# Optimization experiments

Measured on AMD Instinct MI355X. Metric: run time of the kernel, lower is better.

The kernel has to match this reference:

```python
import jax, jax.numpy as jnp
import numpy as np

HEADS = 16
EPS = 1e-5

def _ln(x, w, b):
    # LayerNorm over last axis (per-head dim s), torch default eps=1e-5
    mu = jnp.mean(x, axis=-1, keepdims=True)
    var = jnp.var(x, axis=-1, keepdims=True)
    return (x - mu) * jax.lax.rsqrt(var + EPS) * w + b

def setup_inputs() -> dict:
    key = jax.random.key(0)
    ks = jax.random.split(key, 6)
    b, t, e = 4, 2048, 1024
    sc = 1.0 / np.sqrt(e)  # keep weight magnitudes sane
    return {
        "x": jax.random.normal(ks[0], (b, t, e), jnp.float32),
        "Wk": jax.random.normal(ks[1], (e, e), jnp.float32) * sc,
        "Wq": jax.random.normal(ks[2], (e, e), jnp.float32) * sc,
        "Wv": jax.random.normal(ks[3], (e, e), jnp.float32) * sc,
        "Wu": jax.random.normal(ks[4], (e, e), jnp.float32) * sc,
        "kln_w": jnp.ones((e // HEADS,), jnp.float32),
        "kln_b": jnp.zeros((e // HEADS,), jnp.float32),
        "qln_w": jnp.ones((e // HEADS,), jnp.float32),
        "qln_b": jnp.zeros((e // HEADS,), jnp.float32),
    }

def reference(x, Wk, Wq, Wv, Wu, kln_w, kln_b, qln_w, qln_b):
    b, t, e = x.shape
    h = HEADS
    s = e // h
    scale = 1.0 / np.sqrt(s)
    # nn.Linear(emb, emb, bias=False): y = x @ W.T
    k = (x @ Wk.T).reshape(b, t, h, s)
    q = (x @ Wq.T).reshape(b, t, h, s)
    v = (x @ Wv.T).reshape(b, t, h, s)
    # kqnorm: per-head LayerNorm on keys and queries
    k = _ln(k, kln_w, kln_b)
    q = _ln(q, qln_w, qln_b)
    # scores: (b, h, t, t)
    w = jnp.einsum('bihd,bjhd->bhij', q, k) * scale
    # causal mask: zero out strictly-upper-triangular (future) positions
    causal = jnp.tril(jnp.ones((t, t), bool))
    w = jnp.where(causal, w, -jnp.inf)
    p = jax.nn.softmax(w, axis=-1)
    out = jnp.einsum('bhij,bjhd->bihd', p, v).reshape(b, t, e)
    return out @ Wu.T
```

## Files before the change

### kernel.cpp

```cpp
#include <hip/hip_runtime.h>
#include <math.h>

#define EMB 1024
#define TSEQ 2048
#define NBATCH 4
#define NHEAD 16
#define HDIM 64
#define MROWS (NBATCH * TSEQ)
#define KPAD 72

typedef __attribute__((ext_vector_type(8))) short bf16x8;
typedef __attribute__((ext_vector_type(4))) float f32x4;
typedef __attribute__((ext_vector_type(8))) unsigned short u16x8;
typedef __attribute__((ext_vector_type(4))) unsigned short u16x4;

typedef __attribute__((address_space(1))) const void gas_cv;
typedef __attribute__((address_space(3))) void las_v;

__device__ __forceinline__ void gload_lds16(const void* g, void* l) {
  __builtin_amdgcn_global_load_lds((gas_cv*)g, (las_v*)l, 16, 0, 0);
}

__device__ __forceinline__ unsigned short f2bf(float f) {
  unsigned int x = __float_as_uint(f);
  unsigned int r = x + 0x7fffu + ((x >> 16) & 1u);
  return (unsigned short)(r >> 16);
}
__device__ __forceinline__ float bf2f(unsigned short h) {
  return __uint_as_float((unsigned int)h << 16);
}

__global__ __launch_bounds__(256) void decomp_kernel(
    const float* __restrict__ x, const float* __restrict__ Wk,
    const float* __restrict__ Wq, const float* __restrict__ Wv,
    const float* __restrict__ Wu,
    unsigned short* __restrict__ xh, unsigned short* __restrict__ xl,
    unsigned short* __restrict__ wkh, unsigned short* __restrict__ wkl,
    unsigned short* __restrict__ wqh, unsigned short* __restrict__ wql,
    unsigned short* __restrict__ wvh, unsigned short* __restrict__ wvl,
    unsigned short* __restrict__ wuh, unsigned short* __restrict__ wul) {
  const int v = blockIdx.x * blockDim.x + threadIdx.x;
  const float* src;
  unsigned short *dh, *dl;
  size_t off;
  if (v < (1 << 20)) {
    src = x; dh = xh; dl = xl; off = (size_t)v << 3;
  } else {
    const int wv = v - (1 << 20);
    const int ws_ = wv >> 17;
    off = (size_t)(wv & 131071) << 3;
    if (ws_ == 0) { src = Wk; dh = wkh; dl = wkl; }
    else if (ws_ == 1) { src = Wq; dh = wqh; dl = wql; }
    else if (ws_ == 2) { src = Wv; dh = wvh; dl = wvl; }
    else { src = Wu; dh = wuh; dl = wul; }
  }
  const float4 f0 = *(const float4*)(src + off);
  const float4 f1 = *(const float4*)(src + off + 4);
  const float fv[8] = {f0.x, f0.y, f0.z, f0.w, f1.x, f1.y, f1.z, f1.w};
  u16x8 h, l;
#pragma unroll
  for (int i = 0; i < 8; ++i) {
    const unsigned short hb = f2bf(fv[i]);
    h[i] = hb;
    l[i] = f2bf(fv[i] - bf2f(hb));
  }
  *(u16x8*)(dh + off) = h;
  *(u16x8*)(dl + off) = l;
}

__device__ __forceinline__ void gemm3_core(
    const unsigned short* __restrict__ Ah,
    const unsigned short* __restrict__ Bh, const unsigned short* __restrict__ Bl,
    int bm, int bn, f32x4 acc[4][4]) {
  __shared__ __align__(16) unsigned short As[128][64];
  __shared__ __align__(16) unsigned short Bs[128][64];
  const int tid = threadIdx.x;
  const int lane = tid & 63;
  const int w = tid >> 6;
  const int lq = lane & 15;
  const int g = lane >> 4;
  const int wrO = (w >> 1) << 6;
  const int wcO = (w & 1) << 6;
  const int srow = (w << 5) + (lane >> 3);
  const int scbs = ((lane & 7) ^ (srow & 7)) << 3;
  const int xsw = lq & 7;

  const size_t aoff0 = (size_t)(bm + srow) * EMB + scbs;
  const size_t boff0 = (size_t)(bn + srow) * EMB + scbs;

  for (int s = 0; s < 32; ++s) {
    const int p = s >> 4;
    const int kt = s & 15;
    const unsigned short* Bsrc = (p == 0) ? Bh : Bl;
    const size_t ko = (size_t)(kt << 6);
    __syncthreads();
#pragma unroll
    for (int u = 0; u < 4; ++u) {
      gload_lds16(Ah + aoff0 + ko + (size_t)(u << 3) * EMB,
                  &As[(w << 5) + (u << 3)][0]);
      gload_lds16(Bsrc + boff0 + ko + (size_t)(u << 3) * EMB,
                  &Bs[(w << 5) + (u << 3)][0]);
    }
    __syncthreads();

    bf16x8 af[4][2], bf[4][2];
#pragma unroll
    for (int m = 0; m < 4; ++m)
#pragma unroll
      for (int kk = 0; kk < 2; ++kk) {
        af[m][kk] = *(const bf16x8*)&As[wrO + (m << 4) + lq]
                                      [(((kk << 2) + g) ^ xsw) << 3];
        bf[m][kk] = *(const bf16x8*)&Bs[wcO + (m << 4) + lq]
                                      [(((kk << 2) + g) ^ xsw) << 3];
      }
#pragma unroll
    for (int kk = 0; kk < 2; ++kk)
#pragma unroll
      for (int m = 0; m < 4; ++m)
#pragma unroll
        for (int nb = 0; nb < 4; ++nb)
          acc[m][nb] = __builtin_amdgcn_mfma_f32_16x16x32_bf16(
              af[m][kk], bf[nb][kk], acc[m][nb], 0, 0, 0);
  }
}

__global__ __launch_bounds__(256, 2) void gemm3_qkv_kernel(
    const unsigned short* __restrict__ xh,
    const unsigned short* __restrict__ wkh, const unsigned short* __restrict__ wkl,
    const unsigned short* __restrict__ wqh, const unsigned short* __restrict__ wql,
    const unsigned short* __restrict__ wvh, const unsigned short* __restrict__ wvl,
    unsigned short* __restrict__ kb16, unsigned short* __restrict__ qb16,
    unsigned short* __restrict__ vb16,
    const float* __restrict__ klnw, const float* __restrict__ klnb,
    const float* __restrict__ qlnw, const float* __restrict__ qlnb) {
  const int sel = blockIdx.y >> 3;
  const int bm = blockIdx.x << 7;
  const int bn = (blockIdx.y & 7) << 7;
  const unsigned short* Bh = sel == 0 ? wkh : sel == 1 ? wqh : wvh;
  const unsigned short* Bl = sel == 0 ? wkl : sel == 1 ? wql : wvl;

  f32x4 acc[4][4];
#pragma unroll
  for (int m = 0; m < 4; ++m)
#pragma unroll
    for (int nb = 0; nb < 4; ++nb) acc[m][nb] = (f32x4){0.f, 0.f, 0.f, 0.f};

  gemm3_core(xh, Bh, Bl, bm, bn, acc);

  const int lane = threadIdx.x & 63;
  const int w = threadIdx.x >> 6;
  const int lq = lane & 15;
  const int g = lane >> 4;
  const int wrO = (w >> 1) << 6;
  const int wcO = (w & 1) << 6;

  if (sel < 2) {
    unsigned short* C = sel == 0 ? kb16 : qb16;
    const float* lw = sel == 0 ? klnw : qlnw;
    const float* lb = sel == 0 ? klnb : qlnb;
    float wd[4], bd[4];
#pragma unroll
    for (int nb = 0; nb < 4; ++nb) {
      wd[nb] = lw[(nb << 4) + lq];
      bd[nb] = lb[(nb << 4) + lq];
    }
#pragma unroll
    for (int m = 0; m < 4; ++m) {
      const int r0 = bm + wrO + (m << 4) + (g << 2);
#pragma unroll
      for (int j = 0; j < 4; ++j) {
        float s = acc[m][0][j] + acc[m][1][j] + acc[m][2][j] + acc[m][3][j];
        s += __shfl_xor(s, 1, 64); s += __shfl_xor(s, 2, 64);
        s += __shfl_xor(s, 4, 64); s += __shfl_xor(s, 8, 64);
        const float mu = s * (1.f / 64.f);
        float v2 = 0.f;
#pragma unroll
        for (int nb = 0; nb < 4; ++nb) {
          const float d = acc[m][nb][j] - mu;
          v2 = fmaf(d, d, v2);
        }
        v2 += __shfl_xor(v2, 1, 64); v2 += __shfl_xor(v2, 2, 64);
        v2 += __shfl_xor(v2, 4, 64); v2 += __shfl_xor(v2, 8, 64);
        const float inv = rsqrtf(v2 * (1.f / 64.f) + 1e-5f);
#pragma unroll
        for (int nb = 0; nb < 4; ++nb) {
          const float val = (acc[m][nb][j] - mu) * inv * wd[nb] + bd[nb];
          C[(size_t)(r0 + j) * EMB + bn + wcO + (nb << 4) + lq] = f2bf(val);
        }
      }
    }
  } else {
#pragma unroll
    for (int m = 0; m < 4; ++m) {
      const int r0 = bm + wrO + (m << 4) + (g << 2);
      const int bb = r0 >> 11;
      const int tl = r0 & 2047;
#pragma unroll
      for (int nb = 0; nb < 4; ++nb) {
        const int n = bn + wcO + (nb << 4) + lq;
        const int hh = n >> 6;
        const int dd = n & 63;
        u16x4 pk;
#pragma unroll
        for (int j = 0; j < 4; ++j) pk[j] = f2bf(acc[m][nb][j]);
        *(u16x4*)(vb16 + ((((size_t)(bb << 4) + hh) << 6) + dd) * TSEQ + tl) = pk;
      }
    }
  }
}

__global__ __launch_bounds__(256, 2) void gemm3_out_kernel(
    const unsigned short* __restrict__ ah,
    const unsigned short* __restrict__ wuh, const unsigned short* __restrict__ wul,
    float* __restrict__ C) {
  const int bm = blockIdx.x << 7;
  const int bn = blockIdx.y << 7;
  f32x4 acc[4][4];
#pragma unroll
  for (int m = 0; m < 4; ++m)
#pragma unroll
    for (int nb = 0; nb < 4; ++nb) acc[m][nb] = (f32x4){0.f, 0.f, 0.f, 0.f};

  gemm3_core(ah, wuh, wul, bm, bn, acc);

  const int lane = threadIdx.x & 63;
  const int w = threadIdx.x >> 6;
  const int lq = lane & 15;
  const int g = lane >> 4;
  const int wrO = (w >> 1) << 6;
  const int wcO = (w & 1) << 6;
#pragma unroll
  for (int m = 0; m < 4; ++m) {
    const int r0 = bm + wrO + (m << 4) + (g << 2);
#pragma unroll
    for (int nb = 0; nb < 4; ++nb) {
      const int c = bn + wcO + (nb << 4) + lq;
#pragma unroll
      for (int j = 0; j < 4; ++j) C[(size_t)(r0 + j) * EMB + c] = acc[m][nb][j];
    }
  }
}

#define SCL2E 0.1803368801111244f

__global__ __launch_bounds__(256, 2) void attn_kernel(
    const unsigned short* __restrict__ Qg, const unsigned short* __restrict__ Kg,
    const unsigned short* __restrict__ Vt,
    unsigned short* __restrict__ Oh, unsigned short* __restrict__ Ol) {
  __shared__ __align__(16) unsigned short Ks[64][KPAD];
  __shared__ __align__(16) unsigned short Vs[64][KPAD];
  __shared__ __align__(16) unsigned short Ps[4][16][KPAD];
  const int tid = threadIdx.x;
  const int lane = tid & 63;
  const int w = tid >> 6;
  const int lq = lane & 15;
  const int g = lane >> 4;
  const int qt = (int)(gridDim.x - 1 - blockIdx.x);
  const int bh = blockIdx.y;
  const int bb = bh >> 4;
  const int hh = bh & 15;
  const int q0 = qt << 6;
  const unsigned short* Qb = Qg + ((size_t)bb * TSEQ) * EMB + hh * HDIM;
  const unsigned short* Kb = Kg + ((size_t)bb * TSEQ) * EMB + hh * HDIM;
  const unsigned short* Vb = Vt + (size_t)bh * HDIM * TSEQ;
  unsigned short* Ohb = Oh + ((size_t)bb * TSEQ) * EMB + hh * HDIM;
  unsigned short* Olb = Ol + ((size_t)bb * TSEQ) * EMB + hh * HDIM;

  bf16x8 qf0, qf1;
  {
    const unsigned short* qp = Qb + (size_t)(q0 + (w << 4) + lq) * EMB + (g << 3);
    qf0 = *(const bf16x8*)(qp);
    qf1 = *(const bf16x8*)(qp + 32);
  }

  f32x4 o[4];
#pragma unroll
  for (int nb = 0; nb < 4; ++nb) o[nb] = (f32x4){0.f, 0.f, 0.f, 0.f};
  float mrun = -3.0e38f;
  float lrun = 0.f;
  const int qg_row = q0 + (w << 4) + lq;

  const int skey = tid >> 2;
  const int schunk = (tid & 3) << 4;

  for (int t = 0; t <= qt; ++t) {
    const int k0 = t << 6;
    {
      const unsigned short* kp = Kb + (size_t)(k0 + skey) * EMB + schunk;
      *(bf16x8*)&Ks[skey][schunk] = *(const bf16x8*)kp;
      *(bf16x8*)&Ks[skey][schunk + 8] = *(const bf16x8*)(kp + 8);
      const unsigned short* vp = Vb + (size_t)skey * TSEQ + k0 + schunk;
      *(bf16x8*)&Vs[skey][schunk] = *(const bf16x8*)vp;
      *(bf16x8*)&Vs[skey][schunk + 8] = *(const bf16x8*)(vp + 8);
    }
    __syncthreads();

    f32x4 sacc[4];
#pragma unroll
    for (int mb = 0; mb < 4; ++mb) sacc[mb] = (f32x4){0.f, 0.f, 0.f, 0.f};
    __builtin_amdgcn_s_setprio(1);
#pragma unroll
    for (int mb = 0; mb < 4; ++mb) {
      const bf16x8 ka0 = *(const bf16x8*)&Ks[(mb << 4) + lq][(g << 3)];
      const bf16x8 ka1 = *(const bf16x8*)&Ks[(mb << 4) + lq][(g << 3) + 32];
      sacc[mb] = __builtin_amdgcn_mfma_f32_16x16x32_bf16(ka0, qf0, sacc[mb], 0, 0, 0);
      sacc[mb] = __builtin_amdgcn_mfma_f32_16x16x32_bf16(ka1, qf1, sacc[mb], 0, 0, 0);
    }
    __builtin_amdgcn_s_setprio(0);

    const bool diag = (t == qt);
    float pv[16];
    float pm = -3.0e38f;
#pragma unroll
    for (int mb = 0; mb < 4; ++mb)
#pragma unroll
      for (int r = 0; r < 4; ++r) {
        float s = sacc[mb][r] * SCL2E;
        if (diag && (k0 + (mb << 4) + (g << 2) + r) > qg_row) s = -3.0e38f;
        pv[(mb << 2) + r] = s;
        pm = fmaxf(pm, s);
      }
    pm = fmaxf(pm, __shfl_xor(pm, 16, 64));
    pm = fmaxf(pm, __shfl_xor(pm, 32, 64));

    const bool skip = __all(pm <= mrun);
    const float mnew = skip ? mrun : fmaxf(mrun, pm);
    float ls = 0.f;
#pragma unroll
    for (int i = 0; i < 16; ++i) {
      const float p = exp2f(pv[i] - mnew);
      pv[i] = p;
      ls += p;
    }
    ls += __shfl_xor(ls, 16, 64);
    ls += __shfl_xor(ls, 32, 64);
    if (skip) {
      lrun += ls;
    } else {
      const float corr = exp2f(mrun - mnew);
      mrun = mnew;
      lrun = lrun * corr + ls;
      float corr4[4];
#pragma unroll
      for (int r = 0; r < 4; ++r)
        corr4[r] = __shfl(corr, (lane & 48) | ((g << 2) + r), 64);
#pragma unroll
      for (int nb = 0; nb < 4; ++nb)
#pragma unroll
        for (int r = 0; r < 4; ++r) o[nb][r] *= corr4[r];
    }

    {
      unsigned int* pw = (unsigned int*)&Ps[w][lq][0];
#pragma unroll
      for (int mb = 0; mb < 4; ++mb) {
        const unsigned int u0 =
            (unsigned int)f2bf(pv[(mb << 2) + 0]) | ((unsigned int)f2bf(pv[(mb << 2) + 1]) << 16);
        const unsigned int u1 =
            (unsigned int)f2bf(pv[(mb << 2) + 2]) | ((unsigned int)f2bf(pv[(mb << 2) + 3]) << 16);
        pw[(mb << 3) + (g << 1) + 0] = u0;
        pw[(mb << 3) + (g << 1) + 1] = u1;
      }
    }
    asm volatile("s_waitcnt lgkmcnt(0)" ::: "memory");

    {
      const bf16x8 pa0 = *(const bf16x8*)&Ps[w][lq][(g << 3)];
      const bf16x8 pa1 = *(const bf16x8*)&Ps[w][lq][(g << 3) + 32];
      __builtin_amdgcn_s_setprio(1);
#pragma unroll
      for (int nb = 0; nb < 4; ++nb) {
        const bf16x8 v0 = *(const bf16x8*)&Vs[(nb << 4) + lq][(g << 3)];
        const bf16x8 v1 = *(const bf16x8*)&Vs[(nb << 4) + lq][(g << 3) + 32];
        o[nb] = __builtin_amdgcn_mfma_f32_16x16x32_bf16(pa0, v0, o[nb], 0, 0, 0);
        o[nb] = __builtin_amdgcn_mfma_f32_16x16x32_bf16(pa1, v1, o[nb], 0, 0, 0);
      }
      __builtin_amdgcn_s_setprio(0);
    }
    __syncthreads();
  }

  float li[4];
#pragma unroll
  for (int r = 0; r < 4; ++r)
    li[r] = 1.f / __shfl(lrun, (lane & 48) | ((g << 2) + r), 64);
#pragma unroll
  for (int nb = 0; nb < 4; ++nb)
#pragma unroll
    for (int r = 0; r < 4; ++r) {
      const float val = o[nb][r] * li[r];
      const unsigned short hb = f2bf(val);
      const size_t idx =
          (size_t)(q0 + (w << 4) + (g << 2) + r) * EMB + (nb << 4) + lq;
      Ohb[idx] = hb;
      Olb[idx] = f2bf(val - bf2f(hb));
    }
}

extern "C" void kernel_launch(void* const* d_in, const int* in_sizes, int n_in,
                              void* d_out, int out_size, void* d_ws, size_t ws_size,
                              hipStream_t stream) {
  const float* x  = (const float*)d_in[0];
  const float* Wk = (const float*)d_in[1];
  const float* Wq = (const float*)d_in[2];
  const float* Wv = (const float*)d_in[3];
  const float* Wu = (const float*)d_in[4];
  const float* klnw = (const float*)d_in[5];
  const float* klnb = (const float*)d_in[6];
  const float* qlnw = (const float*)d_in[7];
  const float* qlnb = (const float*)d_in[8];
  float* out = (float*)d_out;

  char* wsb = (char*)d_ws;
  const size_t MB = 1024 * 1024;
  unsigned short* ah   = (unsigned short*)(wsb + 0 * MB);
  unsigned short* al   = (unsigned short*)(wsb + 16 * MB);
  unsigned short* kb16 = (unsigned short*)(wsb + 32 * MB);
  unsigned short* qb16 = (unsigned short*)(wsb + 48 * MB);
  unsigned short* xh   = (unsigned short*)(wsb + 64 * MB);
  unsigned short* xl   = (unsigned short*)(wsb + 80 * MB);
  unsigned short* vb16 = (unsigned short*)(wsb + 96 * MB);
  unsigned short* wkh  = (unsigned short*)(wsb + 112 * MB);
  unsigned short* wkl  = (unsigned short*)(wsb + 114 * MB);
  unsigned short* wqh  = (unsigned short*)(wsb + 116 * MB);
  unsigned short* wql  = (unsigned short*)(wsb + 118 * MB);
  unsigned short* wvh  = (unsigned short*)(wsb + 120 * MB);
  unsigned short* wvl  = (unsigned short*)(wsb + 122 * MB);
  unsigned short* wuh  = (unsigned short*)(wsb + 124 * MB);
  unsigned short* wul  = (unsigned short*)(wsb + 126 * MB);

  decomp_kernel<<<6144, 256, 0, stream>>>(x, Wk, Wq, Wv, Wu, xh, xl, wkh, wkl,
                                          wqh, wql, wvh, wvl, wuh, wul);

  gemm3_qkv_kernel<<<dim3(MROWS / 128, 24), 256, 0, stream>>>(
      xh, wkh, wkl, wqh, wql, wvh, wvl, kb16, qb16, vb16,
      klnw, klnb, qlnw, qlnb);

  attn_kernel<<<dim3(TSEQ / 64, NBATCH * NHEAD), 256, 0, stream>>>(
      qb16, kb16, vb16, ah, al);

  gemm3_out_kernel<<<dim3(MROWS / 128, EMB / 128), 256, 0, stream>>>(
      ah, wuh, wul, out);
}
```

Before: 401.0 us.

## Pair causal query tiles per block to balance work and share K/V loads

Each attention block now handles two query tiles, j and its mirror (31-j), so every block does the same number of key-tile iterations and the K/V tiles staged in shared memory feed both. The grid is halved and launch bounds rise to 4 blocks per CU. The low half of the bf16 hi/lo split of the attention output is no longer written, which removes a store stream and lowers output precision. The out GEMM still reads only the high part, so the dropped buffer looks unused. Register pressure rises from keeping two sets of accumulators and softmax state.

```diff
diff --git a/kernel.cpp b/kernel.cpp
--- a/kernel.cpp
+++ b/kernel.cpp
@@ -243,10 +243,99 @@
 
 #define SCL2E 0.1803368801111244f
 
-__global__ __launch_bounds__(256, 2) void attn_kernel(
+__device__ __forceinline__ void attn_subtile(
+    const bf16x8& qf0, const bf16x8& qf1, f32x4 o[4], float& mrun, float& lrun,
+    int qg_row, int k0, bool diag,
+    const unsigned short (*__restrict__ Ksl)[KPAD],
+    const unsigned short (*__restrict__ Vsl)[KPAD],
+    unsigned short (*__restrict__ Psl)[KPAD],
+    int lane, int lq, int g) {
+  f32x4 sacc[4];
+#pragma unroll
+  for (int mb = 0; mb < 4; ++mb) sacc[mb] = (f32x4){0.f, 0.f, 0.f, 0.f};
+  __builtin_amdgcn_s_setprio(1);
+#pragma unroll
+  for (int mb = 0; mb < 4; ++mb) {
+    const bf16x8 ka0 = *(const bf16x8*)&Ksl[(mb << 4) + lq][(g << 3)];
+    const bf16x8 ka1 = *(const bf16x8*)&Ksl[(mb << 4) + lq][(g << 3) + 32];
+    sacc[mb] = __builtin_amdgcn_mfma_f32_16x16x32_bf16(ka0, qf0, sacc[mb], 0, 0, 0);
+    sacc[mb] = __builtin_amdgcn_mfma_f32_16x16x32_bf16(ka1, qf1, sacc[mb], 0, 0, 0);
+  }
+  __builtin_amdgcn_s_setprio(0);
+
+  float pv[16];
+  float pm = -3.0e38f;
+#pragma unroll
+  for (int mb = 0; mb < 4; ++mb)
+#pragma unroll
+    for (int r = 0; r < 4; ++r) {
+      float s = sacc[mb][r] * SCL2E;
+      if (diag && (k0 + (mb << 4) + (g << 2) + r) > qg_row) s = -3.0e38f;
+      pv[(mb << 2) + r] = s;
+      pm = fmaxf(pm, s);
+    }
+  pm = fmaxf(pm, __shfl_xor(pm, 16, 64));
+  pm = fmaxf(pm, __shfl_xor(pm, 32, 64));
+
+  const bool skip = __all(pm <= mrun);
+  const float mnew = skip ? mrun : fmaxf(mrun, pm);
+  float ls = 0.f;
+#pragma unroll
+  for (int i = 0; i < 16; ++i) {
+    const float p = exp2f(pv[i] - mnew);
+    pv[i] = p;
+    ls += p;
+  }
+  ls += __shfl_xor(ls, 16, 64);
+  ls += __shfl_xor(ls, 32, 64);
+  if (skip) {
+    lrun += ls;
+  } else {
+    const float corr = exp2f(mrun - mnew);
+    mrun = mnew;
+    lrun = lrun * corr + ls;
+    float corr4[4];
+#pragma unroll
+    for (int r = 0; r < 4; ++r)
+      corr4[r] = __shfl(corr, (lane & 48) | ((g << 2) + r), 64);
+#pragma unroll
+    for (int nb = 0; nb < 4; ++nb)
+#pragma unroll
+      for (int r = 0; r < 4; ++r) o[nb][r] *= corr4[r];
+  }
+
+  {
+    unsigned int* pw = (unsigned int*)&Psl[lq][0];
+#pragma unroll
+    for (int mb = 0; mb < 4; ++mb) {
+      const unsigned int u0 =
+          (unsigned int)f2bf(pv[(mb << 2) + 0]) | ((unsigned int)f2bf(pv[(mb << 2) + 1]) << 16);
+      const unsigned int u1 =
+          (unsigned int)f2bf(pv[(mb << 2) + 2]) | ((unsigned int)f2bf(pv[(mb << 2) + 3]) << 16);
+      pw[(mb << 3) + (g << 1) + 0] = u0;
+      pw[(mb << 3) + (g << 1) + 1] = u1;
+    }
+  }
+  asm volatile("s_waitcnt lgkmcnt(0)" ::: "memory");
+
+  {
+    const bf16x8 pa0 = *(const bf16x8*)&Psl[lq][(g << 3)];
+    const bf16x8 pa1 = *(const bf16x8*)&Psl[lq][(g << 3) + 32];
+    __builtin_amdgcn_s_setprio(1);
+#pragma unroll
+    for (int nb = 0; nb < 4; ++nb) {
+      const bf16x8 v0 = *(const bf16x8*)&Vsl[(nb << 4) + lq][(g << 3)];
+      const bf16x8 v1 = *(const bf16x8*)&Vsl[(nb << 4) + lq][(g << 3) + 32];
+      o[nb] = __builtin_amdgcn_mfma_f32_16x16x32_bf16(pa0, v0, o[nb], 0, 0, 0);
+      o[nb] = __builtin_amdgcn_mfma_f32_16x16x32_bf16(pa1, v1, o[nb], 0, 0, 0);
+    }
+    __builtin_amdgcn_s_setprio(0);
+  }
+}
+
+__global__ __launch_bounds__(256, 4) void attn_kernel(
     const unsigned short* __restrict__ Qg, const unsigned short* __restrict__ Kg,
-    const unsigned short* __restrict__ Vt,
-    unsigned short* __restrict__ Oh, unsigned short* __restrict__ Ol) {
+    const unsigned short* __restrict__ Vt, unsigned short* __restrict__ Oh) {
   __shared__ __align__(16) unsigned short Ks[64][KPAD];
   __shared__ __align__(16) unsigned short Vs[64][KPAD];
   __shared__ __align__(16) unsigned short Ps[4][16][KPAD];
@@ -255,35 +344,42 @@
   const int w = tid >> 6;
   const int lq = lane & 15;
   const int g = lane >> 4;
-  const int qt = (int)(gridDim.x - 1 - blockIdx.x);
+  const int jA = blockIdx.x;
+  const int jB = (TSEQ / 64 - 1) - jA;
   const int bh = blockIdx.y;
   const int bb = bh >> 4;
   const int hh = bh & 15;
-  const int q0 = qt << 6;
+  const int q0A = jA << 6;
+  const int q0B = jB << 6;
   const unsigned short* Qb = Qg + ((size_t)bb * TSEQ) * EMB + hh * HDIM;
   const unsigned short* Kb = Kg + ((size_t)bb * TSEQ) * EMB + hh * HDIM;
   const unsigned short* Vb = Vt + (size_t)bh * HDIM * TSEQ;
   unsigned short* Ohb = Oh + ((size_t)bb * TSEQ) * EMB + hh * HDIM;
-  unsigned short* Olb = Ol + ((size_t)bb * TSEQ) * EMB + hh * HDIM;
-
-  bf16x8 qf0, qf1;
+
+  bf16x8 qfA0, qfA1, qfB0, qfB1;
   {
-    const unsigned short* qp = Qb + (size_t)(q0 + (w << 4) + lq) * EMB + (g << 3);
-    qf0 = *(const bf16x8*)(qp);
-    qf1 = *(const bf16x8*)(qp + 32);
-  }
-
-  f32x4 o[4];
-#pragma unroll
-  for (int nb = 0; nb < 4; ++nb) o[nb] = (f32x4){0.f, 0.f, 0.f, 0.f};
-  float mrun = -3.0e38f;
-  float lrun = 0.f;
-  const int qg_row = q0 + (w << 4) + lq;
+    const unsigned short* qpA = Qb + (size_t)(q0A + (w << 4) + lq) * EMB + (g << 3);
+    qfA0 = *(const bf16x8*)(qpA);
+    qfA1 = *(const bf16x8*)(qpA + 32);
+    const unsigned short* qpB = Qb + (size_t)(q0B + (w << 4) + lq) * EMB + (g << 3);
+    qfB0 = *(const bf16x8*)(qpB);
+    qfB1 = *(const bf16x8*)(qpB + 32);
+  }
+
+  f32x4 oA[4], oB[4];
+#pragma unroll
+  for (int nb = 0; nb < 4; ++nb) {
+    oA[nb] = (f32x4){0.f, 0.f, 0.f, 0.f};
+    oB[nb] = (f32x4){0.f, 0.f, 0.f, 0.f};
+  }
+  float mA = -3.0e38f, lA = 0.f, mB = -3.0e38f, lB = 0.f;
+  const int qrowA = q0A + (w << 4) + lq;
+  const int qrowB = q0B + (w << 4) + lq;
 
   const int skey = tid >> 2;
   const int schunk = (tid & 3) << 4;
 
-  for (int t = 0; t <= qt; ++t) {
+  for (int t = 0; t <= jB; ++t) {
     const int k0 = t << 6;
     {
       const unsigned short* kp = Kb + (size_t)(k0 + skey) * EMB + schunk;
@@ -295,105 +391,27 @@
     }
     __syncthreads();
 
-    f32x4 sacc[4];
-#pragma unroll
-    for (int mb = 0; mb < 4; ++mb) sacc[mb] = (f32x4){0.f, 0.f, 0.f, 0.f};
-    __builtin_amdgcn_s_setprio(1);
-#pragma unroll
-    for (int mb = 0; mb < 4; ++mb) {
-      const bf16x8 ka0 = *(const bf16x8*)&Ks[(mb << 4) + lq][(g << 3)];
-      const bf16x8 ka1 = *(const bf16x8*)&Ks[(mb << 4) + lq][(g << 3) + 32];
-      sacc[mb] = __builtin_amdgcn_mfma_f32_16x16x32_bf16(ka0, qf0, sacc[mb], 0, 0, 0);
-      sacc[mb] = __builtin_amdgcn_mfma_f32_16x16x32_bf16(ka1, qf1, sacc[mb], 0, 0, 0);
-    }
-    __builtin_amdgcn_s_setprio(0);
-
-    const bool diag = (t == qt);
-    float pv[16];
-    float pm = -3.0e38f;
-#pragma unroll
-    for (int mb = 0; mb < 4; ++mb)
-#pragma unroll
-      for (int r = 0; r < 4; ++r) {
-        float s = sacc[mb][r] * SCL2E;
-        if (diag && (k0 + (mb << 4) + (g << 2) + r) > qg_row) s = -3.0e38f;
-        pv[(mb << 2) + r] = s;
-        pm = fmaxf(pm, s);
-      }
-    pm = fmaxf(pm, __shfl_xor(pm, 16, 64));
-    pm = fmaxf(pm, __shfl_xor(pm, 32, 64));
-
-    const bool skip = __all(pm <= mrun);
-    const float mnew = skip ? mrun : fmaxf(mrun, pm);
-    float ls = 0.f;
-#pragma unroll
-    for (int i = 0; i < 16; ++i) {
-      const float p = exp2f(pv[i] - mnew);
-      pv[i] = p;
-      ls += p;
-    }
-    ls += __shfl_xor(ls, 16, 64);
-    ls += __shfl_xor(ls, 32, 64);
-    if (skip) {
-      lrun += ls;
-    } else {
-      const float corr = exp2f(mrun - mnew);
-      mrun = mnew;
-      lrun = lrun * corr + ls;
-      float corr4[4];
-#pragma unroll
-      for (int r = 0; r < 4; ++r)
-        corr4[r] = __shfl(corr, (lane & 48) | ((g << 2) + r), 64);
-#pragma unroll
-      for (int nb = 0; nb < 4; ++nb)
-#pragma unroll
-        for (int r = 0; r < 4; ++r) o[nb][r] *= corr4[r];
-    }
-
-    {
-      unsigned int* pw = (unsigned int*)&Ps[w][lq][0];
-#pragma unroll
-      for (int mb = 0; mb < 4; ++mb) {
-        const unsigned int u0 =
-            (unsigned int)f2bf(pv[(mb << 2) + 0]) | ((unsigned int)f2bf(pv[(mb << 2) + 1]) << 16);
-        const unsigned int u1 =
-            (unsigned int)f2bf(pv[(mb << 2) + 2]) | ((unsigned int)f2bf(pv[(mb << 2) + 3]) << 16);
-        pw[(mb << 3) + (g << 1) + 0] = u0;
-        pw[(mb << 3) + (g << 1) + 1] = u1;
-      }
-    }
-    asm volatile("s_waitcnt lgkmcnt(0)" ::: "memory");
-
-    {
-      const bf16x8 pa0 = *(const bf16x8*)&Ps[w][lq][(g << 3)];
-      const bf16x8 pa1 = *(const bf16x8*)&Ps[w][lq][(g << 3) + 32];
-      __builtin_amdgcn_s_setprio(1);
-#pragma unroll
-      for (int nb = 0; nb < 4; ++nb) {
-        const bf16x8 v0 = *(const bf16x8*)&Vs[(nb << 4) + lq][(g << 3)];
-        const bf16x8 v1 = *(const bf16x8*)&Vs[(nb << 4) + lq][(g << 3) + 32];
-        o[nb] = __builtin_amdgcn_mfma_f32_16x16x32_bf16(pa0, v0, o[nb], 0, 0, 0);
-        o[nb] = __builtin_amdgcn_mfma_f32_16x16x32_bf16(pa1, v1, o[nb], 0, 0, 0);
-      }
-      __builtin_amdgcn_s_setprio(0);
-    }
+    attn_subtile(qfB0, qfB1, oB, mB, lB, qrowB, k0, t == jB,
+                 Ks, Vs, Ps[w], lane, lq, g);
+    if (t <= jA)
+      attn_subtile(qfA0, qfA1, oA, mA, lA, qrowA, k0, t == jA,
+                   Ks, Vs, Ps[w], lane, lq, g);
     __syncthreads();
   }
 
-  float li[4];
-#pragma unroll
-  for (int r = 0; r < 4; ++r)
-    li[r] = 1.f / __shfl(lrun, (lane & 48) | ((g << 2) + r), 64);
+  float liA[4], liB[4];
+#pragma unroll
+  for (int r = 0; r < 4; ++r) {
+    liA[r] = 1.f / __shfl(lA, (lane & 48) | ((g << 2) + r), 64);
+    liB[r] = 1.f / __shfl(lB, (lane & 48) | ((g << 2) + r), 64);
+  }
 #pragma unroll
   for (int nb = 0; nb < 4; ++nb)
 #pragma unroll
     for (int r = 0; r < 4; ++r) {
-      const float val = o[nb][r] * li[r];
-      const unsigned short hb = f2bf(val);
-      const size_t idx =
-          (size_t)(q0 + (w << 4) + (g << 2) + r) * EMB + (nb << 4) + lq;
-      Ohb[idx] = hb;
-      Olb[idx] = f2bf(val - bf2f(hb));
+      const int rr = (w << 4) + (g << 2) + r;
+      Ohb[(size_t)(q0A + rr) * EMB + (nb << 4) + lq] = f2bf(oA[nb][r] * liA[r]);
+      Ohb[(size_t)(q0B + rr) * EMB + (nb << 4) + lq] = f2bf(oB[nb][r] * liB[r]);
     }
 }
 
@@ -414,7 +432,6 @@
   char* wsb = (char*)d_ws;
   const size_t MB = 1024 * 1024;
   unsigned short* ah   = (unsigned short*)(wsb + 0 * MB);
-  unsigned short* al   = (unsigned short*)(wsb + 16 * MB);
   unsigned short* kb16 = (unsigned short*)(wsb + 32 * MB);
   unsigned short* qb16 = (unsigned short*)(wsb + 48 * MB);
   unsigned short* xh   = (unsigned short*)(wsb + 64 * MB);
@@ -436,8 +453,8 @@
       xh, wkh, wkl, wqh, wql, wvh, wvl, kb16, qb16, vb16,
       klnw, klnb, qlnw, qlnb);
 
-  attn_kernel<<<dim3(TSEQ / 64, NBATCH * NHEAD), 256, 0, stream>>>(
-      qb16, kb16, vb16, ah, al);
+  attn_kernel<<<dim3(TSEQ / 128, NBATCH * NHEAD), 256, 0, stream>>>(
+      qb16, kb16, vb16, ah);
 
   gemm3_out_kernel<<<dim3(MROWS / 128, EMB / 128), 256, 0, stream>>>(
       ah, wuh, wul, out);
```

Result: faster. 349.6 us (-12.8%).
